# Optimization experiments

Measured on AMD Instinct MI355X. Metric: run time of the kernel, lower is better.

## Reference

```python
import jax, jax.numpy as jnp
import numpy as np

N_NODES = 50000
IN_CH = 128
OUT_CH = 64
N_EDGES = 800000
K_HOPS = 2


def setup_inputs() -> dict:
    key = jax.random.key(0)
    k1, k2, k3, k4 = jax.random.split(key, 4)
    x = jax.random.normal(k1, (N_NODES, IN_CH), dtype=jnp.float32)
    edge_index = jax.random.randint(k2, (2, N_EDGES), 0, N_NODES, dtype=jnp.int64)
    # SGC linear layer params (torch Linear default init approx)
    scale = 1.0 / np.sqrt(IN_CH)
    W = jax.random.uniform(k3, (IN_CH, OUT_CH), dtype=jnp.float32, minval=-scale, maxval=scale)
    b = jax.random.uniform(k4, (OUT_CH,), dtype=jnp.float32, minval=-scale, maxval=scale)
    return {"x": x, "edge_index": edge_index, "W": W, "b": b}


def _sgc_propagate(x, row, col, K):
    # GCN symmetric normalization with self-loops: S = D^-1/2 (A+I) D^-1/2
    n = x.shape[0]
    loop = jnp.arange(n, dtype=row.dtype)
    row = jnp.concatenate([row, loop])
    col = jnp.concatenate([col, loop])
    ones = jnp.ones(row.shape[0], dtype=x.dtype)
    deg = jax.ops.segment_sum(ones, col, num_segments=n)
    dinv = jnp.where(deg > 0, jax.lax.rsqrt(deg), 0.0)
    norm = dinv[row] * dinv[col]  # [E+N]
    for _ in range(K):
        # gather source features, weight, scatter-add to targets
        msg = norm[:, None] * x[row]  # [E+N, C]
        x = jax.ops.segment_sum(msg, col, num_segments=n)
    return x


def reference(x, edge_index, W, b):
    # Dropout is identity in eval mode (deterministic reference).
    row, col = edge_index[0], edge_index[1]
    h = _sgc_propagate(x, row, col, K_HOPS)  # [N, IN_CH]
    return h @ W + b  # [N, OUT_CH]
```

## Files before the change

### kernel.cpp

```cpp
#include <hip/hip_runtime.h>

#define N_NODES 50000
#define IN_CH   128
#define OUT_CH  64
#define N_EDGES 800000
#define NBINS   49
#define LBCAP   128
#define BINCAP  20000
#define PCAP    64
#define WT_STR  136
#define SA_B    500
#define SA_E    1600
#define SB_B    49
#define GEMM_BL 196
#define HOP_NB  782
#define ZPL     (N_NODES * 4)
#define YT_STR  68


using short8  = __attribute__((ext_vector_type(8))) short;
using float4v = __attribute__((ext_vector_type(4))) float;
using uint4v  = __attribute__((ext_vector_type(4))) unsigned int;

__device__ __forceinline__ unsigned int bpack(float a, float b) {
    unsigned int ua = __float_as_uint(a), ub = __float_as_uint(b);
    unsigned int ra = (ua + 0x7fffu + ((ua >> 16) & 1u)) >> 16;
    unsigned int rb = (ub + 0x7fffu + ((ub >> 16) & 1u)) & 0xffff0000u;
    return (ra & 0xffffu) | rb;
}

__global__ __launch_bounds__(256) void scatter_a(const int* __restrict__ row,
        const int* __restrict__ col, unsigned int* __restrict__ binbuf,
        int* __restrict__ gcur) {
    __shared__ unsigned int sbuf[NBINS][LBCAP];
    __shared__ int scnt[NBINS];
    __shared__ int sdst[NBINS];
    const int tid = threadIdx.x;
    if (tid < NBINS) scnt[tid] = 0;
    __syncthreads();
    const int e0 = blockIdx.x * SA_E;
    for (int i = tid; i < SA_E / 4; i += 256) {
        int e = e0 + i * 4;
        int4 t4 = *(const int4*)&col[e];
        int4 s4 = *(const int4*)&row[e];
        const int ts[4] = { t4.x, t4.y, t4.z, t4.w };
        const int ss[4] = { s4.x, s4.y, s4.z, s4.w };
        #pragma unroll
        for (int j = 0; j < 4; ++j) {
            int b = ts[j] >> 10;
            int pos = atomicAdd(&scnt[b], 1);
            if (pos < LBCAP)
                sbuf[b][pos] = ((unsigned)(ts[j] & 1023) << 16) | (unsigned)ss[j];
        }
    }
    __syncthreads();
    if (tid < NBINS) {
        int c = scnt[tid]; if (c > LBCAP) c = LBCAP; scnt[tid] = c;
        sdst[tid] = atomicAdd(&gcur[tid], c);
    }
    __syncthreads();
    const int wave = tid >> 6, lane = tid & 63;
    for (int b = wave; b < NBINS; b += 4) {
        int c = scnt[b];
        size_t d = (size_t)b * BINCAP + sdst[b];
        for (int i = lane; i < c; i += 64)
            binbuf[d + i] = sbuf[b][i];
    }
}

__global__ __launch_bounds__(1024) void deg_count(
        const unsigned int* __restrict__ binbuf, const int* __restrict__ gcur,
        int* __restrict__ deg32) {
    __shared__ int lcnt[1024];
    const int bid = blockIdx.x, tid = threadIdx.x;
    lcnt[tid] = 0;
    __syncthreads();
    int cnt = gcur[bid]; if (cnt > BINCAP) cnt = BINCAP;
    const unsigned int* src = binbuf + (size_t)bid * BINCAP;
    for (int i = tid; i < cnt; i += 1024)
        atomicAdd(&lcnt[src[i] >> 16], 1);
    __syncthreads();
    int t = (bid << 10) + tid;
    if (t < N_NODES) deg32[t] = lcnt[tid];
}

__global__ __launch_bounds__(1024) void scatb_gemm(
        const unsigned int* __restrict__ binbuf, const int* __restrict__ gcur,
        unsigned short* __restrict__ esrc, const int* __restrict__ deg32,
        const float* __restrict__ x, const float* __restrict__ W,
        uint4v* __restrict__ z0) {
    const int bid = blockIdx.x, tid = threadIdx.x;
    if (bid < SB_B) {
        __shared__ int lcnt[1024];
        const int t0 = bid << 10;
        lcnt[tid] = 0;
        __syncthreads();
        int cnt = gcur[bid]; if (cnt > BINCAP) cnt = BINCAP;
        const unsigned int* src = binbuf + (size_t)bid * BINCAP;
        for (int i = tid; i < cnt; i += 1024) {
            unsigned int e = src[i];
            int tl = e >> 16;
            int pos = atomicAdd(&lcnt[tl], 1);
            int t = t0 + tl;
            if (pos < PCAP && t < N_NODES)
                esrc[(size_t)pos * N_NODES + t] = (unsigned short)(e & 0xffffu);
        }
        return;
    }
    __shared__ unsigned short sWT[64 * WT_STR];
    __shared__ float ytile[16 * 16 * YT_STR];
    for (int i = tid; i < IN_CH * OUT_CH; i += 1024) {
        int k = i >> 6, c = i & 63;
        unsigned int u = __float_as_uint(W[i]);
        u = (u + 0x7fffu + ((u >> 16) & 1u)) >> 16;
        sWT[c * WT_STR + k] = (unsigned short)u;
    }
    __syncthreads();
    const int lane = tid & 63;
    const int quad = lane >> 4;
    const int c15  = lane & 15;
    const int wid  = tid >> 6;
    const int tile = (bid - SB_B) * 16 + wid;
    if (tile >= N_NODES / 16) return;

    short8 bf[4][4];
    #pragma unroll
    for (int t = 0; t < 4; ++t)
        #pragma unroll
        for (int ch = 0; ch < 4; ++ch)
            bf[ch][t] = *(const short8*)&sWT[(t * 16 + c15) * WT_STR + ch * 32 + quad * 8];

    const float* xr = x + ((size_t)tile * 16 + c15) * IN_CH;
    float4v acc[4] = {{0.f,0.f,0.f,0.f},{0.f,0.f,0.f,0.f},
                      {0.f,0.f,0.f,0.f},{0.f,0.f,0.f,0.f}};
    #pragma unroll
    for (int ch = 0; ch < 4; ++ch) {
        float4 f0 = *(const float4*)(xr + ch * 32 + quad * 8);
        float4 f1 = *(const float4*)(xr + ch * 32 + quad * 8 + 4);
        unsigned int d0 = bpack(f0.x, f0.y), d1 = bpack(f0.z, f0.w);
        unsigned int d2 = bpack(f1.x, f1.y), d3 = bpack(f1.z, f1.w);
        short8 a8;
        a8[0] = (short)d0; a8[1] = (short)(d0 >> 16);
        a8[2] = (short)d1; a8[3] = (short)(d1 >> 16);
        a8[4] = (short)d2; a8[5] = (short)(d2 >> 16);
        a8[6] = (short)d3; a8[7] = (short)(d3 >> 16);
        #pragma unroll
        for (int t = 0; t < 4; ++t)
            acc[t] = __builtin_amdgcn_mfma_f32_16x16x32_bf16(a8, bf[ch][t], acc[t], 0, 0, 0);
    }
    float* yt = &ytile[wid * (16 * YT_STR)];
    #pragma unroll
    for (int t = 0; t < 4; ++t)
        #pragma unroll
        for (int r = 0; r < 4; ++r)
            yt[(quad * 4 + r) * YT_STR + t * 16 + c15] = acc[t][r];
    #pragma unroll
    for (int k = 0; k < 2; ++k) {
        int u = lane + 64 * k;
        int node = u >> 3, j = u & 7;
        int half = j >> 2, qq = j & 3;
        const float* src = &yt[node * YT_STR + j * 8];
        float4 f0 = *(const float4*)src;
        float4 f1 = *(const float4*)(src + 4);
        int n = tile * 16 + node;
        float dv = rsqrtf((float)(deg32[n] + 1));
        uint4v pk;
        pk.x = bpack(dv * f0.x, dv * f0.y);
        pk.y = bpack(dv * f0.z, dv * f0.w);
        pk.z = bpack(dv * f1.x, dv * f1.y);
        pk.w = bpack(dv * f1.z, dv * f1.w);
        __builtin_nontemporal_store(pk, z0 + (size_t)half * ZPL + (size_t)n * 4 + qq);
    }
}

__global__ __launch_bounds__(256) void hop_gather(const uint4v* __restrict__ hin,
        void* __restrict__ hout, const int* __restrict__ deg32,
        const unsigned short* __restrict__ esrc, const float* __restrict__ bias,
        int last) {
    const int half = blockIdx.x & 1;
    const int wg   = blockIdx.x >> 1;
    const int lane = threadIdx.x & 63;
    const int r    = lane >> 2;
    const int q    = lane & 3;
    const int t    = wg * 64 + (threadIdx.x >> 6) * 16 + r;
    if (t >= N_NODES) return;
    int deg = deg32[t]; if (deg > PCAP) deg = PCAP;
    const uint4v* hp = hin + (size_t)half * ZPL;

    uint4v rr = hp[t * 4 + q];
    float acc[8];
    {
        const unsigned int rw[4] = { rr.x, rr.y, rr.z, rr.w };
        #pragma unroll
        for (int j = 0; j < 4; ++j) {
            acc[2 * j]     = __uint_as_float(rw[j] << 16);
            acc[2 * j + 1] = __uint_as_float(rw[j] & 0xffff0000u);
        }
    }
    int e = 0;
    int s = (0 < deg) ? (int)esrc[t] : -1;
    while (__any(s >= 0)) {
        int sn = (e + 1 < deg) ? (int)esrc[(size_t)(e + 1) * N_NODES + t] : -1;
        if (s >= 0) {
            uint4v v = hp[s * 4 + q];
            const unsigned int rw[4] = { v.x, v.y, v.z, v.w };
            #pragma unroll
            for (int j = 0; j < 4; ++j) {
                acc[2 * j]     += __uint_as_float(rw[j] << 16);
                acc[2 * j + 1] += __uint_as_float(rw[j] & 0xffff0000u);
            }
        }
        s = sn; ++e;
    }

    if (!last) {
        float rdeg = 1.0f / (float)(deg + 1);
        uint4v pk;
        pk.x = bpack(acc[0] * rdeg, acc[1] * rdeg);
        pk.y = bpack(acc[2] * rdeg, acc[3] * rdeg);
        pk.z = bpack(acc[4] * rdeg, acc[5] * rdeg);
        pk.w = bpack(acc[6] * rdeg, acc[7] * rdeg);
        __builtin_nontemporal_store(pk,
            (uint4v*)hout + (size_t)half * ZPL + t * 4 + q);
    } else {
        float d = rsqrtf((float)(deg + 1));
        float4 b0 = ((const float4*)bias)[half * 8 + q * 2];
        float4 b1 = ((const float4*)bias)[half * 8 + q * 2 + 1];
        float4v o0 = { d * acc[0] + b0.x, d * acc[1] + b0.y,
                       d * acc[2] + b0.z, d * acc[3] + b0.w };
        float4v o1 = { d * acc[4] + b1.x, d * acc[5] + b1.y,
                       d * acc[6] + b1.z, d * acc[7] + b1.w };
        __builtin_nontemporal_store(o0, (float4v*)hout + t * 16 + half * 8 + q * 2);
        __builtin_nontemporal_store(o1, (float4v*)hout + t * 16 + half * 8 + q * 2 + 1);
    }
}

extern "C" void kernel_launch(void* const* d_in, const int* in_sizes, int n_in,
                              void* d_out, int out_size, void* d_ws, size_t ws_size,
                              hipStream_t stream) {
    const float* x  = (const float*)d_in[0];
    const int*   ei = (const int*)d_in[1];
    const float* W  = (const float*)d_in[2];
    const float* b  = (const float*)d_in[3];
    float*       out = (float*)d_out;

    const int* row = ei;
    const int* col = ei + N_EDGES;

    char* ws = (char*)d_ws;
    size_t a = 0;
    auto alloc = [&](size_t bytes) { char* p = ws + a; a = (a + bytes + 255) & ~(size_t)255; return p; };
    int*            gcur   = (int*)           alloc(NBINS * sizeof(int));
    int*            deg32  = (int*)           alloc((size_t)N_NODES * sizeof(int));
    unsigned int*   binbuf = (unsigned int*)  alloc((size_t)NBINS * BINCAP * 4);
    unsigned short* esrc   = (unsigned short*)alloc((size_t)PCAP * N_NODES * 2);
    unsigned int*   z0     = (unsigned int*)  alloc((size_t)N_NODES * OUT_CH * 2);
    unsigned int*   z1     = (unsigned int*)  alloc((size_t)N_NODES * OUT_CH * 2);

    hipMemsetAsync(gcur, 0, NBINS * sizeof(int), stream);

    const int B = 256;
    int gH = 2 * HOP_NB;

    scatter_a<<<SA_B, B, 0, stream>>>(row, col, binbuf, gcur);
    deg_count<<<NBINS, 1024, 0, stream>>>(binbuf, gcur, deg32);
    scatb_gemm<<<SB_B + GEMM_BL, 1024, 0, stream>>>(binbuf, gcur, esrc, deg32, x, W,
                                                    (uint4v*)z0);
    hop_gather<<<gH, B, 0, stream>>>((const uint4v*)z0, (void*)z1, deg32, esrc, b, 0);
    hop_gather<<<gH, B, 0, stream>>>((const uint4v*)z1, (void*)out, deg32, esrc, b, 1);
}
```

Measured before the change: 150.8 us.

## Sort nodes by degree within bins to balance hop gather wavefronts

The scatter-B stage now bucket-sorts the nodes of each 1024-node bin by in-degree. It writes an order permutation and a byte degree array, and lays out the edge-source slots by sorted position. The hop gather kernels then map each thread group to a sorted slot, so nodes of similar degree share a wavefront. This is meant to cut the divergent `__any` loop iterations spent waiting on the highest-degree lane. In exchange, the hop kernels do one extra indirection through the order array, and their output stores become scattered by node.

```diff
diff --git a/kernel.cpp b/kernel.cpp
--- a/kernel.cpp
+++ b/kernel.cpp
@@ -16,6 +16,7 @@
 #define HOP_NB  782
 #define ZPL     (N_NODES * 4)
 #define YT_STR  68
+#define SLOTPAD 50176
 
 
 using short8  = __attribute__((ext_vector_type(8))) short;
@@ -87,12 +88,34 @@
 __global__ __launch_bounds__(1024) void scatb_gemm(
         const unsigned int* __restrict__ binbuf, const int* __restrict__ gcur,
         unsigned short* __restrict__ esrc, const int* __restrict__ deg32,
+        int* __restrict__ order, unsigned char* __restrict__ sdeg,
         const float* __restrict__ x, const float* __restrict__ W,
         uint4v* __restrict__ z0) {
     const int bid = blockIdx.x, tid = threadIdx.x;
     if (bid < SB_B) {
         __shared__ int lcnt[1024];
+        __shared__ int slotl[1024];
+        __shared__ int bkt[66];
         const int t0 = bid << 10;
+        const int t = t0 + tid;
+        int mydeg = (t < N_NODES) ? deg32[t] : -1;
+        if (tid < 66) bkt[tid] = 0;
+        __syncthreads();
+        int d = (mydeg < 0) ? 65 : (mydeg > 64 ? 64 : mydeg);
+        atomicAdd(&bkt[d], 1);
+        __syncthreads();
+        if (tid == 0) {
+            int run = 0;
+            for (int i = 0; i < 66; ++i) { int c = bkt[i]; bkt[i] = run; run += c; }
+        }
+        __syncthreads();
+        int sl = atomicAdd(&bkt[d], 1);
+        slotl[tid] = sl;
+        if (mydeg >= 0) {
+            order[t0 + sl] = t;
+            sdeg[t0 + sl] = (unsigned char)(mydeg > 255 ? 255 : mydeg);
+        }
+        __syncthreads();
         lcnt[tid] = 0;
         __syncthreads();
         int cnt = gcur[bid]; if (cnt > BINCAP) cnt = BINCAP;
@@ -101,9 +124,9 @@
             unsigned int e = src[i];
             int tl = e >> 16;
             int pos = atomicAdd(&lcnt[tl], 1);
-            int t = t0 + tl;
-            if (pos < PCAP && t < N_NODES)
-                esrc[(size_t)pos * N_NODES + t] = (unsigned short)(e & 0xffffu);
+            if (pos < PCAP)
+                esrc[(size_t)pos * N_NODES + (t0 + slotl[tl])] =
+                    (unsigned short)(e & 0xffffu);
         }
         return;
     }
@@ -159,9 +182,9 @@
         int u = lane + 64 * k;
         int node = u >> 3, j = u & 7;
         int half = j >> 2, qq = j & 3;
-        const float* src = &yt[node * YT_STR + j * 8];
-        float4 f0 = *(const float4*)src;
-        float4 f1 = *(const float4*)(src + 4);
+        const float* srcp = &yt[node * YT_STR + j * 8];
+        float4 f0 = *(const float4*)srcp;
+        float4 f1 = *(const float4*)(srcp + 4);
         int n = tile * 16 + node;
         float dv = rsqrtf((float)(deg32[n] + 1));
         uint4v pk;
@@ -174,20 +197,22 @@
 }
 
 __global__ __launch_bounds__(256) void hop_gather(const uint4v* __restrict__ hin,
-        void* __restrict__ hout, const int* __restrict__ deg32,
-        const unsigned short* __restrict__ esrc, const float* __restrict__ bias,
-        int last) {
+        void* __restrict__ hout, const unsigned char* __restrict__ sdeg,
+        const int* __restrict__ order, const unsigned short* __restrict__ esrc,
+        const float* __restrict__ bias, int last) {
     const int half = blockIdx.x & 1;
     const int wg   = blockIdx.x >> 1;
     const int lane = threadIdx.x & 63;
     const int r    = lane >> 2;
     const int q    = lane & 3;
-    const int t    = wg * 64 + (threadIdx.x >> 6) * 16 + r;
-    if (t >= N_NODES) return;
-    int deg = deg32[t]; if (deg > PCAP) deg = PCAP;
+    const int slot = wg * 64 + (threadIdx.x >> 6) * 16 + r;
+    if (slot >= N_NODES) return;
+    const int node = order[slot];
+    int dg = sdeg[slot];
+    int deg = dg > PCAP ? PCAP : dg;
     const uint4v* hp = hin + (size_t)half * ZPL;
 
-    uint4v rr = hp[t * 4 + q];
+    uint4v rr = hp[node * 4 + q];
     float acc[8];
     {
         const unsigned int rw[4] = { rr.x, rr.y, rr.z, rr.w };
@@ -198,9 +223,9 @@
         }
     }
     int e = 0;
-    int s = (0 < deg) ? (int)esrc[t] : -1;
+    int s = (0 < deg) ? (int)esrc[slot] : -1;
     while (__any(s >= 0)) {
-        int sn = (e + 1 < deg) ? (int)esrc[(size_t)(e + 1) * N_NODES + t] : -1;
+        int sn = (e + 1 < deg) ? (int)esrc[(size_t)(e + 1) * N_NODES + slot] : -1;
         if (s >= 0) {
             uint4v v = hp[s * 4 + q];
             const unsigned int rw[4] = { v.x, v.y, v.z, v.w };
@@ -221,7 +246,7 @@
         pk.z = bpack(acc[4] * rdeg, acc[5] * rdeg);
         pk.w = bpack(acc[6] * rdeg, acc[7] * rdeg);
         __builtin_nontemporal_store(pk,
-            (uint4v*)hout + (size_t)half * ZPL + t * 4 + q);
+            (uint4v*)hout + (size_t)half * ZPL + (size_t)node * 4 + q);
     } else {
         float d = rsqrtf((float)(deg + 1));
         float4 b0 = ((const float4*)bias)[half * 8 + q * 2];
@@ -230,8 +255,10 @@
                        d * acc[2] + b0.z, d * acc[3] + b0.w };
         float4v o1 = { d * acc[4] + b1.x, d * acc[5] + b1.y,
                        d * acc[6] + b1.z, d * acc[7] + b1.w };
-        __builtin_nontemporal_store(o0, (float4v*)hout + t * 16 + half * 8 + q * 2);
-        __builtin_nontemporal_store(o1, (float4v*)hout + t * 16 + half * 8 + q * 2 + 1);
+        __builtin_nontemporal_store(o0,
+            (float4v*)hout + (size_t)node * 16 + half * 8 + q * 2);
+        __builtin_nontemporal_store(o1,
+            (float4v*)hout + (size_t)node * 16 + half * 8 + q * 2 + 1);
     }
 }
 
@@ -252,6 +279,8 @@
     auto alloc = [&](size_t bytes) { char* p = ws + a; a = (a + bytes + 255) & ~(size_t)255; return p; };
     int*            gcur   = (int*)           alloc(NBINS * sizeof(int));
     int*            deg32  = (int*)           alloc((size_t)N_NODES * sizeof(int));
+    int*            order  = (int*)           alloc((size_t)SLOTPAD * sizeof(int));
+    unsigned char*  sdeg   = (unsigned char*) alloc(SLOTPAD);
     unsigned int*   binbuf = (unsigned int*)  alloc((size_t)NBINS * BINCAP * 4);
     unsigned short* esrc   = (unsigned short*)alloc((size_t)PCAP * N_NODES * 2);
     unsigned int*   z0     = (unsigned int*)  alloc((size_t)N_NODES * OUT_CH * 2);
@@ -264,8 +293,8 @@
 
     scatter_a<<<SA_B, B, 0, stream>>>(row, col, binbuf, gcur);
     deg_count<<<NBINS, 1024, 0, stream>>>(binbuf, gcur, deg32);
-    scatb_gemm<<<SB_B + GEMM_BL, 1024, 0, stream>>>(binbuf, gcur, esrc, deg32, x, W,
-                                                    (uint4v*)z0);
-    hop_gather<<<gH, B, 0, stream>>>((const uint4v*)z0, (void*)z1, deg32, esrc, b, 0);
-    hop_gather<<<gH, B, 0, stream>>>((const uint4v*)z1, (void*)out, deg32, esrc, b, 1);
-}
+    scatb_gemm<<<SB_B + GEMM_BL, 1024, 0, stream>>>(binbuf, gcur, esrc, deg32,
+                                                    order, sdeg, x, W, (uint4v*)z0);
+    hop_gather<<<gH, B, 0, stream>>>((const uint4v*)z0, (void*)z1, sdeg, order, esrc, b, 0);
+    hop_gather<<<gH, B, 0, stream>>>((const uint4v*)z1, (void*)out, sdeg, order, esrc, b, 1);
+}
```

After: 150.9 us. No clear change (+0.1%).
